# Performance work log

Measured on AMD Instinct MI355X. Metric: run time of the kernel, lower is better.

## Reference

```python
import jax, jax.numpy as jnp
import numpy as np

B, S, D = 2, 2048, 1024
H, HKV, DK = 16, 4, 64          # n_heads, n_kv_heads, head dim
NREP = H // HKV                  # 4


def apply_rope(x):
    # Faithful to the original: positions run over x.shape[-2], which is the
    # HEAD axis (x is [B, S, H, DK]) due to how the torch module is written.
    d = x.shape[-1]
    h = x.shape[-2]
    inv_freq = 1.0 / (10000.0 ** (jnp.arange(0, d, 2, dtype=jnp.float32) / d))
    freqs = jnp.arange(h, dtype=jnp.float32)[:, None] * inv_freq[None, :]  # [H, DK/2]
    cos, sin = jnp.cos(freqs), jnp.sin(freqs)
    x1, x2 = x[..., 0::2], x[..., 1::2]
    # interleave back: stack on new last axis then flatten
    return jnp.stack([x1 * cos - x2 * sin, x1 * sin + x2 * cos], axis=-1).reshape(x.shape)


def setup_inputs() -> dict:
    key = jax.random.key(0)
    kx, kq, kk, kv, ko = jax.random.split(key, 5)
    std = 0.02
    x = jax.random.normal(kx, (B, S, D), jnp.float32)
    w_q = jax.random.normal(kq, (D, H * DK), jnp.float32) * std
    w_k = jax.random.normal(kk, (D, HKV * DK), jnp.float32) * std
    w_v = jax.random.normal(kv, (D, HKV * DK), jnp.float32) * std
    w_o = jax.random.normal(ko, (D, D), jnp.float32) * std
    # causal mask, broadcastable to [B, H, S, S]
    mask = jnp.tril(jnp.ones((S, S), bool))[None, None]  # [1,1,S,S]
    return {"x": x, "w_q": w_q, "w_k": w_k, "w_v": w_v, "w_o": w_o, "mask": mask}


def reference(x, w_q, w_k, w_v, w_o, mask):
    b, s, d = x.shape
    Q = (x @ w_q).reshape(b, s, H, DK)
    K = (x @ w_k).reshape(b, s, HKV, DK)
    V = (x @ w_v).reshape(b, s, HKV, DK)
    Q = apply_rope(Q)
    K = apply_rope(K)
    # [B,H,S,DK] with query heads grouped per kv head (matches repeat_interleave)
    Q = Q.transpose(0, 2, 1, 3).reshape(b, HKV, NREP, s, DK)
    K = K.transpose(0, 2, 1, 3)  # [B,HKV,S,DK]
    V = V.transpose(0, 2, 1, 3)
    scores = jnp.einsum('bgrqd,bgkd->bgrqk', Q, K) / np.float32(np.sqrt(DK))
    scores = scores.astype(jnp.float32)
    neg = jnp.finfo(jnp.float32).min
    scores = jnp.where(mask[:, :, None, :, :], scores, neg)  # [1,1,1,S,S] broadcast
    w = jax.nn.softmax(scores, axis=-1)
    ctx = jnp.einsum('bgrqk,bgkd->bgrqd', w, V)  # [B,HKV,NREP,S,DK]
    ctx = ctx.reshape(b, H, s, DK).transpose(0, 2, 1, 3).reshape(b, s, d)
    return ctx @ w_o
```

## Files before the change

### kernel.cpp

```cpp
#include <hip/hip_runtime.h>
#include <hip/hip_bf16.h>

#define S_LEN 2048
#define NBATCH 2
#define DMODEL 1024
#define NHEAD 16
#define NKV 4
#define HDIM 64

typedef __attribute__((ext_vector_type(4))) float f32x4;
typedef __attribute__((ext_vector_type(8))) short s16x8;

#define QSCALE 0.18033688011112042f

__device__ __forceinline__ unsigned short f32_bf16(float f) {
    unsigned int u = __float_as_uint(f);
    u += 0x7FFFu + ((u >> 16) & 1u);
    return (unsigned short)(u >> 16);
}

__global__ __launch_bounds__(256) void cvt_bf16_k(const float* __restrict__ in,
                                                  unsigned short* __restrict__ out, int n4) {
    int i = blockIdx.x * 256 + threadIdx.x;
    if (i < n4) {
        const float4 v = reinterpret_cast<const float4*>(in)[i];
        ushort4 r;
        r.x = f32_bf16(v.x); r.y = f32_bf16(v.y);
        r.z = f32_bf16(v.z); r.w = f32_bf16(v.w);
        reinterpret_cast<ushort4*>(out)[i] = r;
    }
}

__global__ __launch_bounds__(256) void cvtT_k(const float* __restrict__ in,
                                              unsigned short* __restrict__ out,
                                              int N, int n_off) {
    __shared__ float t[64][65];
    const int n0  = blockIdx.x * 64;
    const int k0  = blockIdx.y * 64;
    const int tid = threadIdx.x;
    const int r   = tid >> 4;
    const int c4  = (tid & 15) * 4;
    #pragma unroll
    for (int i = 0; i < 4; ++i) {
        const float4 v = *reinterpret_cast<const float4*>(
            in + (size_t)(k0 + i*16 + r) * N + n0 + c4);
        t[i*16 + r][c4+0] = v.x; t[i*16 + r][c4+1] = v.y;
        t[i*16 + r][c4+2] = v.z; t[i*16 + r][c4+3] = v.w;
    }
    __syncthreads();
    #pragma unroll
    for (int i = 0; i < 4; ++i) {
        const int n = i*16 + r;
        ushort4 o;
        o.x = f32_bf16(t[c4+0][n]); o.y = f32_bf16(t[c4+1][n]);
        o.z = f32_bf16(t[c4+2][n]); o.w = f32_bf16(t[c4+3][n]);
        *reinterpret_cast<ushort4*>(out + (size_t)(n_off + n0 + n) * 1024 + k0 + c4) = o;
    }
}

using gas_u32 = const unsigned int __attribute__((address_space(1))) *;
using las_u32 = unsigned int __attribute__((address_space(3))) *;

template<int EPI>
__global__ __launch_bounds__(256, 3) void gemm2_k(
    const unsigned short* __restrict__ A,
    const unsigned short* __restrict__ Bt,
    int N, int K,
    float* __restrict__ OutF,
    unsigned short* __restrict__ Qb,
    unsigned short* __restrict__ Kbuf,
    unsigned short* __restrict__ Vbuf)
{
    __shared__ unsigned short As[2][128 * 64];
    __shared__ unsigned short Bs[2][64 * 64];

    const int tid  = threadIdx.x;
    const int lane = tid & 63;
    const int l15  = lane & 15;
    const int l4   = lane >> 4;
    const int wave = tid >> 6;
    const int wm   = wave >> 1;
    const int wn   = wave & 1;
    const int bm   = blockIdx.y * 128;
    const int bn   = blockIdx.x * 64;

    f32x4 acc[4][2] = {};

    const int NT = K >> 6;

    #define GSTAGE(buf, k0)                                                        \
        {                                                                          \
            _Pragma("unroll")                                                      \
            for (int p = 0; p < 4; ++p) {                                          \
                const int c = p*256 + tid, r_ = c >> 3;                            \
                const int nc = (c & 7) ^ (r_ & 7);                                 \
                __builtin_amdgcn_global_load_lds(                                  \
                    (gas_u32)(A + (size_t)(bm + r_) * K + (k0) + nc*8),            \
                    (las_u32)(&As[buf][c*8]), 16, 0, 0);                           \
            }                                                                      \
            _Pragma("unroll")                                                      \
            for (int p = 0; p < 2; ++p) {                                          \
                const int c = p*256 + tid, r_ = c >> 3;                            \
                const int nc = (c & 7) ^ (r_ & 7);                                 \
                __builtin_amdgcn_global_load_lds(                                  \
                    (gas_u32)(Bt + (size_t)(bn + r_) * K + (k0) + nc*8),           \
                    (las_u32)(&Bs[buf][c*8]), 16, 0, 0);                           \
            }                                                                      \
        }

    GSTAGE(0, 0); __syncthreads();

    for (int kt = 0; kt < NT; ++kt) {
        const int cur = kt & 1;
        if (kt + 1 < NT) GSTAGE(cur ^ 1, (kt + 1) << 6);
        #pragma unroll
        for (int ks = 0; ks < 2; ++ks) {
            s16x8 af[4], bfv[2];
            #pragma unroll
            for (int mi = 0; mi < 4; ++mi) {
                const int r = wm*64 + mi*16 + l15;
                af[mi] = *reinterpret_cast<const s16x8*>(
                    &As[cur][r*64 + (((ks*4 + l4) ^ (r & 7)) * 8)]);
            }
            #pragma unroll
            for (int nj = 0; nj < 2; ++nj) {
                const int r = wn*32 + nj*16 + l15;
                bfv[nj] = *reinterpret_cast<const s16x8*>(
                    &Bs[cur][r*64 + (((ks*4 + l4) ^ (r & 7)) * 8)]);
            }
            #pragma unroll
            for (int mi = 0; mi < 4; ++mi)
                #pragma unroll
                for (int nj = 0; nj < 2; ++nj)
                    acc[mi][nj] = __builtin_amdgcn_mfma_f32_16x16x32_bf16(
                        af[mi], bfv[nj], acc[mi][nj], 0, 0, 0);
        }
        __syncthreads();
    }
    #undef GSTAGE

    #pragma unroll
    for (int mi = 0; mi < 4; ++mi) {
        #pragma unroll
        for (int nj = 0; nj < 2; ++nj) {
            #pragma unroll
            for (int v = 0; v < 4; ++v) {
                const int gr = bm + wm*64 + mi*16 + l4*4 + v;
                const int gc = bn + wn*32 + nj*16 + l15;
                float val = acc[mi][nj][v];
                if (EPI == 0) {
                    OutF[(size_t)gr * N + gc] = val;
                } else {
                    const int b  = gr >> 11;
                    const int sr = gr & (S_LEN - 1);
                    const int dk = gc & 63;
                    if (bn < 1024) {
                        const float partner = __shfl_xor(val, 1, 64);
                        const int   jp  = dk >> 1;
                        const float inv = __expf((float)jp * (-2.0f / 64.0f) * 9.210340371976184f);
                        const int   hh  = gc >> 6;
                        float sn, cs;
                        __sincosf((float)hh * inv, &sn, &cs);
                        val = ((gc & 1) == 0) ? (val * cs - partner * sn)
                                              : (partner * sn + val * cs);
                        val *= QSCALE;
                        Qb[(((size_t)b * NHEAD + hh) * S_LEN + sr) * HDIM + dk] = f32_bf16(val);
                    } else if (bn < 1280) {
                        const float partner = __shfl_xor(val, 1, 64);
                        const int   jp  = dk >> 1;
                        const float inv = __expf((float)jp * (-2.0f / 64.0f) * 9.210340371976184f);
                        const int   hh  = (gc - 1024) >> 6;
                        float sn, cs;
                        __sincosf((float)hh * inv, &sn, &cs);
                        val = ((gc & 1) == 0) ? (val * cs - partner * sn)
                                              : (partner * sn + val * cs);
                        Kbuf[(((size_t)b * NKV + hh) * S_LEN + sr) * HDIM + dk] = f32_bf16(val);
                    } else {
                        const int hh = (gc - 1280) >> 6;
                        Vbuf[(((size_t)b * NKV + hh) * HDIM + dk) * S_LEN + sr] = f32_bf16(val);
                    }
                }
            }
        }
    }
}


__device__ __forceinline__ void stage_load(
    const unsigned short* __restrict__ Kp,
    const unsigned short* __restrict__ Vp,
    int kv0, int tid, s16x8& kr, s16x8& vr)
{
    const int r = tid >> 3, col = (tid & 7) * 8;
    kr = *reinterpret_cast<const s16x8*>(Kp + (size_t)(kv0 + r) * HDIM + col);
    vr = *reinterpret_cast<const s16x8*>(Vp + (size_t)r * S_LEN + kv0 + col);
}

__device__ __forceinline__ void stage_write(
    unsigned short (*Ksb)[72], unsigned short (*Vsb)[72],
    int tid, const s16x8& kr, const s16x8& vr)
{
    const int r = tid >> 3, col = (tid & 7) * 8;
    *reinterpret_cast<s16x8*>(&Ksb[r][col]) = kr;
    *reinterpret_cast<s16x8*>(&Vsb[r][col]) = vr;
}

template<bool MASK>
__device__ __forceinline__ void attn_compute(
    int l15, int l4, int wloc,
    const unsigned short (*Ksb)[72], const unsigned short (*Vsb)[72],
    const s16x8 qf[2], f32x4 o[4], float& m, float& lsum,
    unsigned short (*Plds)[72])
{
    f32x4 s[4] = {};
    __builtin_amdgcn_s_setprio(1);
    #pragma unroll
    for (int c = 0; c < 4; ++c)
        #pragma unroll
        for (int ks = 0; ks < 2; ++ks) {
            const s16x8 kf = *reinterpret_cast<const s16x8*>(&Ksb[c*16 + l15][ks*32 + l4*8]);
            s[c] = __builtin_amdgcn_mfma_f32_16x16x32_bf16(kf, qf[ks], s[c], 0, 0, 0);
        }
    __builtin_amdgcn_s_setprio(0);

    if (MASK) {
        const int qloc = wloc + l15;
        #pragma unroll
        for (int c = 0; c < 4; ++c)
            #pragma unroll
            for (int v = 0; v < 4; ++v) {
                const int kvloc = c*16 + l4*4 + v;
                s[c][v] = (kvloc <= qloc) ? s[c][v] : -1e30f;
            }
    }

    float mx = -1e30f;
    #pragma unroll
    for (int c = 0; c < 4; ++c)
        #pragma unroll
        for (int v = 0; v < 4; ++v) mx = fmaxf(mx, s[c][v]);
    mx = fmaxf(mx, __shfl_xor(mx, 16, 64));
    mx = fmaxf(mx, __shfl_xor(mx, 32, 64));
    if (!__all(mx <= m + 8.0f)) {
        const float mnew  = fmaxf(m, mx);
        const float scale = __builtin_amdgcn_exp2f(m - mnew);
        lsum *= scale;
        #pragma unroll
        for (int dkc = 0; dkc < 4; ++dkc) o[dkc] *= scale;
        m = mnew;
    }
    float psum = 0.0f;
    #pragma unroll
    for (int c = 0; c < 4; ++c)
        #pragma unroll
        for (int v = 0; v < 4; ++v) {
            const float p = __builtin_amdgcn_exp2f(s[c][v] - m);
            s[c][v] = p;
            psum += p;
        }
    lsum += psum;

    #pragma unroll
    for (int c = 0; c < 4; ++c) {
        uint2 w;
        w.x = (unsigned int)f32_bf16(s[c][0]) | ((unsigned int)f32_bf16(s[c][1]) << 16);
        w.y = (unsigned int)f32_bf16(s[c][2]) | ((unsigned int)f32_bf16(s[c][3]) << 16);
        *reinterpret_cast<uint2*>(&Plds[l15][c*16 + l4*4]) = w;
    }
    s16x8 pb[2];
    #pragma unroll
    for (int ks = 0; ks < 2; ++ks)
        pb[ks] = *reinterpret_cast<const s16x8*>(&Plds[l15][ks*32 + l4*8]);

    __builtin_amdgcn_s_setprio(1);
    #pragma unroll
    for (int dkc = 0; dkc < 4; ++dkc)
        #pragma unroll
        for (int ks = 0; ks < 2; ++ks) {
            const s16x8 vf = *reinterpret_cast<const s16x8*>(&Vsb[dkc*16 + l15][ks*32 + l4*8]);
            o[dkc] = __builtin_amdgcn_mfma_f32_16x16x32_bf16(vf, pb[ks], o[dkc], 0, 0, 0);
        }
    __builtin_amdgcn_s_setprio(0);
}

__global__ __launch_bounds__(512, 2) void attn_k(
    const unsigned short* __restrict__ Q,
    const unsigned short* __restrict__ Kb,
    const unsigned short* __restrict__ Vt,
    unsigned short* __restrict__ Ctx)
{
    __shared__ unsigned short Ks[2][64][72];
    __shared__ unsigned short Vs[2][64][72];
    __shared__ unsigned short Plds[8][16][72];

    const int tid  = threadIdx.x;
    const int lane = tid & 63;
    const int l15  = lane & 15;
    const int l4   = lane >> 4;
    const int wave = tid >> 6;

    const int L  = blockIdx.x;
    const int h  = L & 15;
    const int b  = (L >> 4) & 1;
    const int p  = (L >> 5) & 7;
    const int qt = (L < 256) ? (15 - p) : p;
    const int qb0 = qt * 128;

    const int g   = h >> 2;

    const unsigned short* Qp = Q  + ((size_t)b * NHEAD + h) * S_LEN * HDIM;
    const unsigned short* Kp = Kb + ((size_t)b * NKV  + g) * S_LEN * HDIM;
    const unsigned short* Vp = Vt + ((size_t)b * NKV  + g) * HDIM * S_LEN;

    const int qb = qb0 + wave * 16;
    const int dt = qb >> 6;
    const int NT = qt * 2 + 2;

    s16x8 qf[2];
    #pragma unroll
    for (int ks = 0; ks < 2; ++ks)
        qf[ks] = *reinterpret_cast<const s16x8*>(Qp + (size_t)(qb + l15) * HDIM + ks*32 + l4*8);

    f32x4 o[4] = {};
    float m = -1e30f, lsum = 0.0f;

    {
        s16x8 kr, vr;
        stage_load(Kp, Vp, 0, tid, kr, vr);
        stage_write(Ks[0], Vs[0], tid, kr, vr);
        __syncthreads();
    }

    for (int t = 0; t < NT; ++t) {
        const int cur = t & 1;
        s16x8 kr, vr;
        const bool more = (t + 1 < NT);
        if (more) stage_load(Kp, Vp, (t + 1) * 64, tid, kr, vr);
        if (t < dt)
            attn_compute<false>(l15, l4, wave*16 - t*64 + qb0, Ks[cur], Vs[cur], qf, o, m, lsum, Plds[wave]);
        else if (t == dt)
            attn_compute<true >(l15, l4, wave*16 - t*64 + qb0, Ks[cur], Vs[cur], qf, o, m, lsum, Plds[wave]);
        if (more) stage_write(Ks[cur ^ 1], Vs[cur ^ 1], tid, kr, vr);
        __syncthreads();
    }

    lsum += __shfl_xor(lsum, 16, 64);
    lsum += __shfl_xor(lsum, 32, 64);
    const float inv = 1.0f / lsum;
    unsigned short* cp = Ctx + (((size_t)b * S_LEN + qb + l15) * NHEAD + h) * HDIM;
    #pragma unroll
    for (int dkc = 0; dkc < 4; ++dkc) {
        ushort4 r;
        r.x = f32_bf16(o[dkc][0] * inv);
        r.y = f32_bf16(o[dkc][1] * inv);
        r.z = f32_bf16(o[dkc][2] * inv);
        r.w = f32_bf16(o[dkc][3] * inv);
        *reinterpret_cast<ushort4*>(cp + dkc*16 + l4*4) = r;
    }
}

extern "C" void kernel_launch(void* const* d_in, const int* in_sizes, int n_in,
                              void* d_out, int out_size, void* d_ws, size_t ws_size,
                              hipStream_t stream) {
    const float* x  = (const float*)d_in[0];
    const float* wq = (const float*)d_in[1];
    const float* wk = (const float*)d_in[2];
    const float* wv = (const float*)d_in[3];
    const float* wo = (const float*)d_in[4];
    float* out = (float*)d_out;

    const int M  = NBATCH * S_LEN;
    const int nX = M * DMODEL;
    const int nQ = NBATCH * NHEAD * S_LEN * HDIM;
    const int nKV = NBATCH * NKV * S_LEN * HDIM;

    unsigned short* xb    = (unsigned short*)d_ws;
    unsigned short* Wqkvt = xb + nX;
    unsigned short* Wot   = Wqkvt + 1536 * 1024;
    unsigned short* Qb    = Wot + 1024 * 1024;
    unsigned short* Kb    = Qb + nQ;
    unsigned short* Vbuf  = Kb + nKV;
    unsigned short* Ctx   = xb;

    cvt_bf16_k<<<nX / 1024, 256, 0, stream>>>(x, xb, nX / 4);
    cvtT_k<<<dim3(16, 16), 256, 0, stream>>>(wq, Wqkvt, 1024, 0);
    cvtT_k<<<dim3( 4, 16), 256, 0, stream>>>(wk, Wqkvt,  256, 1024);
    cvtT_k<<<dim3( 4, 16), 256, 0, stream>>>(wv, Wqkvt,  256, 1280);
    cvtT_k<<<dim3(16, 16), 256, 0, stream>>>(wo, Wot,   1024, 0);

    gemm2_k<1><<<dim3(1536/64, M/128), 256, 0, stream>>>(
        xb, Wqkvt, 1536, DMODEL, nullptr, Qb, Kb, Vbuf);

    attn_k<<<dim3(512, 1, 1), 512, 0, stream>>>(Qb, Kb, Vbuf, Ctx);

    gemm2_k<0><<<dim3(DMODEL/64, M/128), 256, 0, stream>>>(
        Ctx, Wot, DMODEL, DMODEL, out, nullptr, nullptr, nullptr);
}
```

Before: 104.8 us.

## Process 32 query rows per wave to reuse K/V LDS fragments across two tiles

Result: slower. 121.7 us (+16.1%).

```diff
diff --git a/kernel.cpp b/kernel.cpp
--- a/kernel.cpp
+++ b/kernel.cpp
@@ -189,51 +189,33 @@
 __device__ __forceinline__ void stage_load(
     const unsigned short* __restrict__ Kp,
     const unsigned short* __restrict__ Vp,
-    int kv0, int tid, s16x8& kr, s16x8& vr)
-{
-    const int r = tid >> 3, col = (tid & 7) * 8;
-    kr = *reinterpret_cast<const s16x8*>(Kp + (size_t)(kv0 + r) * HDIM + col);
-    vr = *reinterpret_cast<const s16x8*>(Vp + (size_t)r * S_LEN + kv0 + col);
+    int kv0, int tid, s16x8 (&kr)[2], s16x8 (&vr)[2])
+{
+    #pragma unroll
+    for (int cc = 0; cc < 2; ++cc) {
+        const int c = cc * 256 + tid;
+        const int r = c >> 3, col = (c & 7) * 8;
+        kr[cc] = *reinterpret_cast<const s16x8*>(Kp + (size_t)(kv0 + r) * HDIM + col);
+        vr[cc] = *reinterpret_cast<const s16x8*>(Vp + (size_t)r * S_LEN + kv0 + col);
+    }
 }
 
 __device__ __forceinline__ void stage_write(
     unsigned short (*Ksb)[72], unsigned short (*Vsb)[72],
-    int tid, const s16x8& kr, const s16x8& vr)
-{
-    const int r = tid >> 3, col = (tid & 7) * 8;
-    *reinterpret_cast<s16x8*>(&Ksb[r][col]) = kr;
-    *reinterpret_cast<s16x8*>(&Vsb[r][col]) = vr;
-}
-
-template<bool MASK>
-__device__ __forceinline__ void attn_compute(
-    int l15, int l4, int wloc,
-    const unsigned short (*Ksb)[72], const unsigned short (*Vsb)[72],
-    const s16x8 qf[2], f32x4 o[4], float& m, float& lsum,
-    unsigned short (*Plds)[72])
-{
-    f32x4 s[4] = {};
-    __builtin_amdgcn_s_setprio(1);
-    #pragma unroll
-    for (int c = 0; c < 4; ++c)
-        #pragma unroll
-        for (int ks = 0; ks < 2; ++ks) {
-            const s16x8 kf = *reinterpret_cast<const s16x8*>(&Ksb[c*16 + l15][ks*32 + l4*8]);
-            s[c] = __builtin_amdgcn_mfma_f32_16x16x32_bf16(kf, qf[ks], s[c], 0, 0, 0);
-        }
-    __builtin_amdgcn_s_setprio(0);
-
-    if (MASK) {
-        const int qloc = wloc + l15;
-        #pragma unroll
-        for (int c = 0; c < 4; ++c)
-            #pragma unroll
-            for (int v = 0; v < 4; ++v) {
-                const int kvloc = c*16 + l4*4 + v;
-                s[c][v] = (kvloc <= qloc) ? s[c][v] : -1e30f;
-            }
-    }
-
+    int tid, const s16x8 (&kr)[2], const s16x8 (&vr)[2])
+{
+    #pragma unroll
+    for (int cc = 0; cc < 2; ++cc) {
+        const int c = cc * 256 + tid;
+        const int r = c >> 3, col = (c & 7) * 8;
+        *reinterpret_cast<s16x8*>(&Ksb[r][col]) = kr[cc];
+        *reinterpret_cast<s16x8*>(&Vsb[r][col]) = vr[cc];
+    }
+}
+
+__device__ __forceinline__ void softmax_update(
+    f32x4 (&s)[4], f32x4 (&o)[4], float& m, float& lsum)
+{
     float mx = -1e30f;
     #pragma unroll
     for (int c = 0; c < 4; ++c)
@@ -259,18 +241,61 @@
             psum += p;
         }
     lsum += psum;
+}
+
+template<bool MASK>
+__device__ __forceinline__ void attn_compute32(
+    int l15, int l4, int wloc,
+    const unsigned short (*Ksb)[72], const unsigned short (*Vsb)[72],
+    const s16x8 qf0[2], const s16x8 qf1[2],
+    f32x4 (&o0)[4], f32x4 (&o1)[4],
+    float& m0, float& m1, float& lsum0, float& lsum1,
+    unsigned short (*Plds)[72])
+{
+    f32x4 s0[4] = {}, s1[4] = {};
+    __builtin_amdgcn_s_setprio(1);
+    #pragma unroll
+    for (int c = 0; c < 4; ++c)
+        #pragma unroll
+        for (int ks = 0; ks < 2; ++ks) {
+            const s16x8 kf = *reinterpret_cast<const s16x8*>(&Ksb[c*16 + l15][ks*32 + l4*8]);
+            s0[c] = __builtin_amdgcn_mfma_f32_16x16x32_bf16(kf, qf0[ks], s0[c], 0, 0, 0);
+            s1[c] = __builtin_amdgcn_mfma_f32_16x16x32_bf16(kf, qf1[ks], s1[c], 0, 0, 0);
+        }
+    __builtin_amdgcn_s_setprio(0);
+
+    if (MASK) {
+        const int q0 = wloc + l15;
+        const int q1 = wloc + 16 + l15;
+        #pragma unroll
+        for (int c = 0; c < 4; ++c)
+            #pragma unroll
+            for (int v = 0; v < 4; ++v) {
+                const int kvloc = c*16 + l4*4 + v;
+                s0[c][v] = (kvloc <= q0) ? s0[c][v] : -1e30f;
+                s1[c][v] = (kvloc <= q1) ? s1[c][v] : -1e30f;
+            }
+    }
+
+    softmax_update(s0, o0, m0, lsum0);
+    softmax_update(s1, o1, m1, lsum1);
 
     #pragma unroll
     for (int c = 0; c < 4; ++c) {
-        uint2 w;
-        w.x = (unsigned int)f32_bf16(s[c][0]) | ((unsigned int)f32_bf16(s[c][1]) << 16);
-        w.y = (unsigned int)f32_bf16(s[c][2]) | ((unsigned int)f32_bf16(s[c][3]) << 16);
-        *reinterpret_cast<uint2*>(&Plds[l15][c*16 + l4*4]) = w;
-    }
-    s16x8 pb[2];
-    #pragma unroll
-    for (int ks = 0; ks < 2; ++ks)
-        pb[ks] = *reinterpret_cast<const s16x8*>(&Plds[l15][ks*32 + l4*8]);
+        uint2 w0, w1;
+        w0.x = (unsigned int)f32_bf16(s0[c][0]) | ((unsigned int)f32_bf16(s0[c][1]) << 16);
+        w0.y = (unsigned int)f32_bf16(s0[c][2]) | ((unsigned int)f32_bf16(s0[c][3]) << 16);
+        w1.x = (unsigned int)f32_bf16(s1[c][0]) | ((unsigned int)f32_bf16(s1[c][1]) << 16);
+        w1.y = (unsigned int)f32_bf16(s1[c][2]) | ((unsigned int)f32_bf16(s1[c][3]) << 16);
+        *reinterpret_cast<uint2*>(&Plds[l15][c*16 + l4*4])      = w0;
+        *reinterpret_cast<uint2*>(&Plds[16 + l15][c*16 + l4*4]) = w1;
+    }
+    s16x8 pb0[2], pb1[2];
+    #pragma unroll
+    for (int ks = 0; ks < 2; ++ks) {
+        pb0[ks] = *reinterpret_cast<const s16x8*>(&Plds[l15][ks*32 + l4*8]);
+        pb1[ks] = *reinterpret_cast<const s16x8*>(&Plds[16 + l15][ks*32 + l4*8]);
+    }
 
     __builtin_amdgcn_s_setprio(1);
     #pragma unroll
@@ -278,12 +303,13 @@
         #pragma unroll
         for (int ks = 0; ks < 2; ++ks) {
             const s16x8 vf = *reinterpret_cast<const s16x8*>(&Vsb[dkc*16 + l15][ks*32 + l4*8]);
-            o[dkc] = __builtin_amdgcn_mfma_f32_16x16x32_bf16(vf, pb[ks], o[dkc], 0, 0, 0);
+            o0[dkc] = __builtin_amdgcn_mfma_f32_16x16x32_bf16(vf, pb0[ks], o0[dkc], 0, 0, 0);
+            o1[dkc] = __builtin_amdgcn_mfma_f32_16x16x32_bf16(vf, pb1[ks], o1[dkc], 0, 0, 0);
         }
     __builtin_amdgcn_s_setprio(0);
 }
 
-__global__ __launch_bounds__(512, 2) void attn_k(
+__global__ __launch_bounds__(256, 2) void attn_k(
     const unsigned short* __restrict__ Q,
     const unsigned short* __restrict__ Kb,
     const unsigned short* __restrict__ Vt,
@@ -291,7 +317,7 @@
 {
     __shared__ unsigned short Ks[2][64][72];
     __shared__ unsigned short Vs[2][64][72];
-    __shared__ unsigned short Plds[8][16][72];
+    __shared__ unsigned short Plds[4][32][72];
 
     const int tid  = threadIdx.x;
     const int lane = tid & 63;
@@ -312,20 +338,22 @@
     const unsigned short* Kp = Kb + ((size_t)b * NKV  + g) * S_LEN * HDIM;
     const unsigned short* Vp = Vt + ((size_t)b * NKV  + g) * HDIM * S_LEN;
 
-    const int qb = qb0 + wave * 16;
+    const int qb = qb0 + wave * 32;
     const int dt = qb >> 6;
     const int NT = qt * 2 + 2;
 
-    s16x8 qf[2];
-    #pragma unroll
-    for (int ks = 0; ks < 2; ++ks)
-        qf[ks] = *reinterpret_cast<const s16x8*>(Qp + (size_t)(qb + l15) * HDIM + ks*32 + l4*8);
-
-    f32x4 o[4] = {};
-    float m = -1e30f, lsum = 0.0f;
+    s16x8 qf0[2], qf1[2];
+    #pragma unroll
+    for (int ks = 0; ks < 2; ++ks) {
+        qf0[ks] = *reinterpret_cast<const s16x8*>(Qp + (size_t)(qb + l15)      * HDIM + ks*32 + l4*8);
+        qf1[ks] = *reinterpret_cast<const s16x8*>(Qp + (size_t)(qb + 16 + l15) * HDIM + ks*32 + l4*8);
+    }
+
+    f32x4 o0[4] = {}, o1[4] = {};
+    float m0 = -1e30f, m1 = -1e30f, lsum0 = 0.0f, lsum1 = 0.0f;
 
     {
-        s16x8 kr, vr;
+        s16x8 kr[2], vr[2];
         stage_load(Kp, Vp, 0, tid, kr, vr);
         stage_write(Ks[0], Vs[0], tid, kr, vr);
         __syncthreads();
@@ -333,29 +361,36 @@
 
     for (int t = 0; t < NT; ++t) {
         const int cur = t & 1;
-        s16x8 kr, vr;
+        s16x8 kr[2], vr[2];
         const bool more = (t + 1 < NT);
         if (more) stage_load(Kp, Vp, (t + 1) * 64, tid, kr, vr);
         if (t < dt)
-            attn_compute<false>(l15, l4, wave*16 - t*64 + qb0, Ks[cur], Vs[cur], qf, o, m, lsum, Plds[wave]);
+            attn_compute32<false>(l15, l4, qb - t*64, Ks[cur], Vs[cur],
+                                  qf0, qf1, o0, o1, m0, m1, lsum0, lsum1, Plds[wave]);
         else if (t == dt)
-            attn_compute<true >(l15, l4, wave*16 - t*64 + qb0, Ks[cur], Vs[cur], qf, o, m, lsum, Plds[wave]);
+            attn_compute32<true >(l15, l4, qb - t*64, Ks[cur], Vs[cur],
+                                  qf0, qf1, o0, o1, m0, m1, lsum0, lsum1, Plds[wave]);
         if (more) stage_write(Ks[cur ^ 1], Vs[cur ^ 1], tid, kr, vr);
         __syncthreads();
     }
 
-    lsum += __shfl_xor(lsum, 16, 64);
-    lsum += __shfl_xor(lsum, 32, 64);
-    const float inv = 1.0f / lsum;
-    unsigned short* cp = Ctx + (((size_t)b * S_LEN + qb + l15) * NHEAD + h) * HDIM;
+    lsum0 += __shfl_xor(lsum0, 16, 64);
+    lsum0 += __shfl_xor(lsum0, 32, 64);
+    lsum1 += __shfl_xor(lsum1, 16, 64);
+    lsum1 += __shfl_xor(lsum1, 32, 64);
+    const float inv0 = 1.0f / lsum0;
+    const float inv1 = 1.0f / lsum1;
+    unsigned short* cp0 = Ctx + (((size_t)b * S_LEN + qb + l15)      * NHEAD + h) * HDIM;
+    unsigned short* cp1 = Ctx + (((size_t)b * S_LEN + qb + 16 + l15) * NHEAD + h) * HDIM;
     #pragma unroll
     for (int dkc = 0; dkc < 4; ++dkc) {
-        ushort4 r;
-        r.x = f32_bf16(o[dkc][0] * inv);
-        r.y = f32_bf16(o[dkc][1] * inv);
-        r.z = f32_bf16(o[dkc][2] * inv);
-        r.w = f32_bf16(o[dkc][3] * inv);
-        *reinterpret_cast<ushort4*>(cp + dkc*16 + l4*4) = r;
+        ushort4 r0, r1;
+        r0.x = f32_bf16(o0[dkc][0] * inv0); r0.y = f32_bf16(o0[dkc][1] * inv0);
+        r0.z = f32_bf16(o0[dkc][2] * inv0); r0.w = f32_bf16(o0[dkc][3] * inv0);
+        r1.x = f32_bf16(o1[dkc][0] * inv1); r1.y = f32_bf16(o1[dkc][1] * inv1);
+        r1.z = f32_bf16(o1[dkc][2] * inv1); r1.w = f32_bf16(o1[dkc][3] * inv1);
+        *reinterpret_cast<ushort4*>(cp0 + dkc*16 + l4*4) = r0;
+        *reinterpret_cast<ushort4*>(cp1 + dkc*16 + l4*4) = r1;
     }
 }
 
@@ -391,7 +426,7 @@
     gemm2_k<1><<<dim3(1536/64, M/128), 256, 0, stream>>>(
         xb, Wqkvt, 1536, DMODEL, nullptr, Qb, Kb, Vbuf);
 
-    attn_k<<<dim3(512, 1, 1), 512, 0, stream>>>(Qb, Kb, Vbuf, Ctx);
+    attn_k<<<dim3(512, 1, 1), 256, 0, stream>>>(Qb, Kb, Vbuf, Ctx);
 
     gemm2_k<0><<<dim3(DMODEL/64, M/128), 256, 0, stream>>>(
         Ctx, Wot, DMODEL, DMODEL, out, nullptr, nullptr, nullptr);
```
